# Optimization experiments

Measured on AMD Instinct MI355X. Metric: run time of the kernel, lower is better.

Reference implementation:

```python
import jax, jax.numpy as jnp
import numpy as np

MARGIN = 0.2
EPS = 1e-5
NEG_SENTINEL = -1e9


def _cos_sim(a, b):
    a = a / jnp.linalg.norm(a, axis=-1, keepdims=True)
    b = b / jnp.linalg.norm(b, axis=-1, keepdims=True)
    return a @ b.T  # [B, B]


def _row_losses(sm, labels):
    # sm: [B, B] similarity matrix; one loop body of the original, vectorized over rows i.
    diag = jnp.diagonal(sm)                      # pos_pair_ (scalar per row)
    pos_valid = diag < (1.0 - EPS)               # pos_pair_[pos_pair_ < 1-eps]
    neg_mask = labels[None, :] != labels[:, None]
    # neg_pair_[neg_pair_ + margin > min(pos_pair_)] ; min of a scalar is itself
    hard = neg_mask & ((sm + MARGIN) > diag[:, None])
    has_neg = jnp.any(hard, axis=1)
    neg_max = jnp.max(jnp.where(hard, sm, NEG_SENTINEL), axis=1)  # max(neg_pair)
    valid = pos_valid & has_neg
    pos_loss = jnp.maximum(0.2 * diag * diag - 0.7 * diag + 0.5, 0.0)
    neg_loss = jnp.maximum(0.9 * neg_max * neg_max - 0.4 * neg_max + 0.03, 0.0)
    return jnp.sum(jnp.where(valid, pos_loss + neg_loss, 0.0))


def setup_inputs() -> dict:
    key = jax.random.key(0)
    k1, k2 = jax.random.split(key)
    B, D = 8192, 256
    audio_embeds = jax.random.normal(k1, (B, D), dtype=jnp.float32)
    text_embeds = jax.random.normal(k2, (B, D), dtype=jnp.float32)
    labels = jnp.arange(B, dtype=jnp.int64)
    return {"audio_embeds": audio_embeds, "text_embeds": text_embeds, "labels": labels}


def reference(audio_embeds, text_embeds, labels):
    scores = _cos_sim(audio_embeds, text_embeds)  # [B, B]
    B = scores.shape[0]
    total = _row_losses(scores, labels) + _row_losses(scores.T, labels)
    return total / B
```

## Files before the change

kernel.cpp:

```cpp
#include <hip/hip_runtime.h>
#include <stdint.h>

#define BM 128
#define BN 128
#define KD 256

typedef __attribute__((ext_vector_type(4))) float f32x4;
typedef __attribute__((ext_vector_type(4))) int   i32x4;
typedef __attribute__((ext_vector_type(8))) int   i32x8;

__global__ __launch_bounds__(256) void norm_kernel(
    const float* __restrict__ a, const float* __restrict__ b,
    unsigned int* __restrict__ an, unsigned int* __restrict__ bn,
    float* __restrict__ diag, float* __restrict__ out, int D) {
  if (blockIdx.x == 0 && threadIdx.x == 0) out[0] = 0.f;
  const int row = blockIdx.x * 4 + (threadIdx.x >> 6);
  const int l = threadIdx.x & 63;
  const float4 av = ((const float4*)(a + (size_t)row * D))[l];
  const float4 bv = ((const float4*)(b + (size_t)row * D))[l];
  float ssa = av.x*av.x + av.y*av.y + av.z*av.z + av.w*av.w;
  float ssb = bv.x*bv.x + bv.y*bv.y + bv.z*bv.z + bv.w*bv.w;
  float dot = av.x*bv.x + av.y*bv.y + av.z*bv.z + av.w*bv.w;
  for (int off = 1; off < 64; off <<= 1) {
    ssa += __shfl_xor(ssa, off, 64);
    ssb += __shfl_xor(ssb, off, 64);
    dot += __shfl_xor(dot, off, 64);
  }
  const float inva = 1.0f / sqrtf(ssa);
  const float invb = 1.0f / sqrtf(ssb);
  if (l == 0) diag[row] = dot * inva * invb;
  int pa = 0, pb = 0;
  pa = __builtin_amdgcn_cvt_pk_fp8_f32(av.x * inva, av.y * inva, pa, 0);
  pa = __builtin_amdgcn_cvt_pk_fp8_f32(av.z * inva, av.w * inva, pa, 1);
  pb = __builtin_amdgcn_cvt_pk_fp8_f32(bv.x * invb, bv.y * invb, pb, 0);
  pb = __builtin_amdgcn_cvt_pk_fp8_f32(bv.z * invb, bv.w * invb, pb, 1);
  an[(size_t)row * (D / 4) + l] = (unsigned int)pa;
  bn[(size_t)row * (D / 4) + l] = (unsigned int)pb;
}

__global__ __launch_bounds__(512, 4) void gemm_max_kernel(
    const unsigned char* __restrict__ an, const unsigned char* __restrict__ bn,
    const int* __restrict__ labels,
    float* __restrict__ row_part, float* __restrict__ col_part, int B) {
  __shared__ __align__(16) unsigned char sA[2][BM * KD];
  __shared__ int lds_lab[8 * BM];
  __shared__ float lds_col[2][BN];

  const int tid  = threadIdx.x;
  const int lane = tid & 63;
  const int w    = tid >> 6;
  const int wm   = w >> 2, wn = w & 3;
  const int g0   = blockIdx.x >> 6;
  const int tj   = blockIdx.x & 63;

  const int sr = lane >> 4;
  const int sc = lane & 15;
  const int fr = lane & 15;
  const int hi = lane >> 4;
  const int p0 = ((2 * hi)     ^ (fr & 7)) * 16;
  const int p1 = ((2 * hi + 1) ^ (fr & 7)) * 16;

  auto stage = [&](int bsel, int k) {
    const int ti = g0 + 8 * k;
    #pragma unroll
    for (int pass = 0; pass < 4; ++pass) {
      const int r0  = pass * 32 + w * 4;
      const int row = r0 + sr;
      const int g = ((sc & 7) ^ (row & 7)) | (sc & 8);
      const unsigned char* ga = an + (size_t)(ti * BM + row) * KD + g * 16;
      __builtin_amdgcn_global_load_lds(
          (const __attribute__((address_space(1))) void*)ga,
          (__attribute__((address_space(3))) void*)(&sA[bsel][r0 * KD + lane * 16]),
          16, 0, 0);
    }
  };

  stage(0, 0);
  #pragma unroll
  for (int h = 0; h < 2; ++h) {
    const int i = h * 512 + tid;
    const int* gl = labels + g0 * 128 + (i >> 7) * 1024 + (i & 127);
    __builtin_amdgcn_global_load_lds(
        (const __attribute__((address_space(1))) void*)gl,
        (__attribute__((address_space(3))) void*)(&lds_lab[h * 512 + w * 64 + lane]),
        4, 0, 0);
  }
  i32x8 bfr[2][2];
  #pragma unroll
  for (int it = 0; it < 2; ++it)
    #pragma unroll
    for (int nt = 0; nt < 2; ++nt) {
      const unsigned char* gb =
          bn + (size_t)(tj * BN + wn * 32 + nt * 16 + fr) * KD + it * 128 + hi * 32;
      bfr[it][nt] = __builtin_shufflevector(*(const i32x4*)gb,
                                            *(const i32x4*)(gb + 16),
                                            0, 1, 2, 3, 4, 5, 6, 7);
    }
  const int labc0 = labels[tj * BN + wn * 32 + fr];
  const int labc1 = labels[tj * BN + wn * 32 + 16 + fr];
  __syncthreads();

  const int SC = 0x7F7F7F7F;
  float cp0 = -1e9f, cp1 = -1e9f;

  #pragma unroll
  for (int k = 0; k < 8; ++k) {
    if (k < 7) stage((k + 1) & 1, k + 1);

    f32x4 acc[4][2];
    #pragma unroll
    for (int mt = 0; mt < 4; ++mt) {
      acc[mt][0] = (f32x4){0.f, 0.f, 0.f, 0.f};
      acc[mt][1] = (f32x4){0.f, 0.f, 0.f, 0.f};
    }
    const unsigned char* Ab = sA[k & 1];
    #pragma unroll
    for (int it = 0; it < 2; ++it)
      #pragma unroll
      for (int mt = 0; mt < 4; ++mt) {
        const unsigned char* ra = Ab + (wm * 64 + mt * 16 + fr) * KD + it * 128;
        i32x8 af = __builtin_shufflevector(*(const i32x4*)(ra + p0),
                                           *(const i32x4*)(ra + p1),
                                           0, 1, 2, 3, 4, 5, 6, 7);
        acc[mt][0] = __builtin_amdgcn_mfma_scale_f32_16x16x128_f8f6f4(
            af, bfr[it][0], acc[mt][0], 0, 0, 0, SC, 0, SC);
        acc[mt][1] = __builtin_amdgcn_mfma_scale_f32_16x16x128_f8f6f4(
            af, bfr[it][1], acc[mt][1], 0, 0, 0, SC, 0, SC);
      }

    const size_t rowbase =
        (size_t)(tj * 4 + wn) * B + (size_t)(g0 + 8 * k) * BM + wm * 64;
    #pragma unroll
    for (int mt = 0; mt < 4; ++mt) {
      const i32x4 lv = *(const i32x4*)&lds_lab[k * 128 + wm * 64 + mt * 16 + hi * 4];
      float rr4[4];
      #pragma unroll
      for (int r = 0; r < 4; ++r) {
        const int l0 = lv[r];
        const float vm0 = (l0 != labc0) ? acc[mt][0][r] : -1e9f;
        const float vm1 = (l0 != labc1) ? acc[mt][1][r] : -1e9f;
        cp0 = fmaxf(cp0, vm0);
        cp1 = fmaxf(cp1, vm1);
        float rm = fmaxf(vm0, vm1);
        rm = fmaxf(rm, __shfl_xor(rm, 1, 64));
        rm = fmaxf(rm, __shfl_xor(rm, 2, 64));
        rm = fmaxf(rm, __shfl_xor(rm, 4, 64));
        rm = fmaxf(rm, __shfl_xor(rm, 8, 64));
        rr4[r] = rm;
      }
      if (fr == mt) {
        f32x4 v = {rr4[0], rr4[1], rr4[2], rr4[3]};
        *(f32x4*)(row_part + rowbase + mt * 16 + hi * 4) = v;
      }
    }

    __syncthreads();
  }

  float c0 = fmaxf(cp0, __shfl_xor(cp0, 16, 64));
  c0 = fmaxf(c0, __shfl_xor(c0, 32, 64));
  float c1 = fmaxf(cp1, __shfl_xor(cp1, 16, 64));
  c1 = fmaxf(c1, __shfl_xor(c1, 32, 64));
  if (hi == 0) {
    lds_col[wm][wn * 32 + fr] = c0;
    lds_col[wm][wn * 32 + 16 + fr] = c1;
  }
  __syncthreads();
  if (tid < BN)
    col_part[(size_t)g0 * B + tj * BN + tid] =
        fmaxf(lds_col[0][tid], lds_col[1][tid]);
}

__global__ __launch_bounds__(256) void finalize_kernel(
    const float* __restrict__ row_part, const float* __restrict__ col_part,
    const float* __restrict__ diag, int B, int Tr, int Tc,
    float* __restrict__ out) {
  const int ln = threadIdx.x & 63;
  const int q  = threadIdx.x >> 6;
  const int item = blockIdx.x * 64 + ln;
  const bool isrow = item < B;
  const int i = isrow ? item : item - B;
  const float* part = isrow ? row_part : col_part;
  const int T = isrow ? Tr : Tc;
  const int tpq = (T + 3) >> 2;
  const int t1 = min(T, (q + 1) * tpq);
  float m = -1e9f;
  for (int t = q * tpq; t < t1; ++t) m = fmaxf(m, part[(size_t)t * B + i]);
  __shared__ float smq[4][64];
  smq[q][ln] = m;
  __syncthreads();
  if (q == 0) {
    m = fmaxf(fmaxf(smq[0][ln], smq[1][ln]), fmaxf(smq[2][ln], smq[3][ln]));
    const float d = diag[i];
    float loss = 0.f;
    if ((d < 1.0f - 1e-5f) && (m + 0.2f > d)) {
      loss = fmaxf(0.2f * d * d - 0.7f * d + 0.5f, 0.f) +
             fmaxf(0.9f * m * m - 0.4f * m + 0.03f, 0.f);
    }
    for (int off = 1; off < 64; off <<= 1) loss += __shfl_xor(loss, off, 64);
    if (ln == 0) atomicAdd(out, loss / (float)B);
  }
}

extern "C" void kernel_launch(void* const* d_in, const int* in_sizes, int n_in,
                              void* d_out, int out_size, void* d_ws, size_t ws_size,
                              hipStream_t stream) {
  const float* a      = (const float*)d_in[0];
  const float* b      = (const float*)d_in[1];
  const int*   labels = (const int*)d_in[2];
  const int B = in_sizes[2];
  const int D = in_sizes[0] / B;
  const int Tr = (B / BN) * 4;
  const int Tc = 8;

  char* ws = (char*)d_ws;
  unsigned char* an = (unsigned char*)ws;
  unsigned char* bn = (unsigned char*)(ws + (size_t)B * D);
  float* diag     = (float*)(ws + (size_t)2 * B * D);
  float* row_part = diag + B;
  float* col_part = row_part + (size_t)Tr * B;

  norm_kernel<<<B / 4, 256, 0, stream>>>(a, b, (unsigned int*)an,
                                         (unsigned int*)bn, diag,
                                         (float*)d_out, D);

  gemm_max_kernel<<<(B / BM) / 8 * (B / BN), 512, 0, stream>>>(
      an, bn, labels, row_part, col_part, B);

  finalize_kernel<<<(2 * B) / 64, 256, 0, stream>>>(
      row_part, col_part, diag, B, Tr, Tc, (float*)d_out);
}
```

Measured before the change: 140.9 us.

## Give each block one output tile and compute the transposed product for row maxima

Each block now handles a single 128x128 tile instead of looping over 8 A-tiles with double-buffered LDS staging, so the grid grows eightfold and column partials cover all B/BM tiles. Row maxima come from a second MFMA that computes the transposed product, so lanes hold rows and need only two shuffles instead of four per element. This drops the per-row shuffle reductions and the double buffering but doubles MFMA work and increases column-partial traffic in finalize.

Result: slower. 153.2 us (+8.7%).

```diff
diff --git a/kernel.cpp b/kernel.cpp
--- a/kernel.cpp
+++ b/kernel.cpp
@@ -42,16 +42,15 @@
     const unsigned char* __restrict__ an, const unsigned char* __restrict__ bn,
     const int* __restrict__ labels,
     float* __restrict__ row_part, float* __restrict__ col_part, int B) {
-  __shared__ __align__(16) unsigned char sA[2][BM * KD];
-  __shared__ int lds_lab[8 * BM];
+  __shared__ __align__(16) unsigned char sA[BM * KD];
   __shared__ float lds_col[2][BN];
 
   const int tid  = threadIdx.x;
   const int lane = tid & 63;
   const int w    = tid >> 6;
   const int wm   = w >> 2, wn = w & 3;
-  const int g0   = blockIdx.x >> 6;
   const int tj   = blockIdx.x & 63;
+  const int ti   = blockIdx.x >> 6;
 
   const int sr = lane >> 4;
   const int sc = lane & 15;
@@ -60,31 +59,18 @@
   const int p0 = ((2 * hi)     ^ (fr & 7)) * 16;
   const int p1 = ((2 * hi + 1) ^ (fr & 7)) * 16;
 
-  auto stage = [&](int bsel, int k) {
-    const int ti = g0 + 8 * k;
-    #pragma unroll
-    for (int pass = 0; pass < 4; ++pass) {
-      const int r0  = pass * 32 + w * 4;
-      const int row = r0 + sr;
-      const int g = ((sc & 7) ^ (row & 7)) | (sc & 8);
-      const unsigned char* ga = an + (size_t)(ti * BM + row) * KD + g * 16;
-      __builtin_amdgcn_global_load_lds(
-          (const __attribute__((address_space(1))) void*)ga,
-          (__attribute__((address_space(3))) void*)(&sA[bsel][r0 * KD + lane * 16]),
-          16, 0, 0);
-    }
-  };
-
-  stage(0, 0);
-  #pragma unroll
-  for (int h = 0; h < 2; ++h) {
-    const int i = h * 512 + tid;
-    const int* gl = labels + g0 * 128 + (i >> 7) * 1024 + (i & 127);
+  #pragma unroll
+  for (int pass = 0; pass < 4; ++pass) {
+    const int r0  = pass * 32 + w * 4;
+    const int row = r0 + sr;
+    const int g = ((sc & 7) ^ (row & 7)) | (sc & 8);
+    const unsigned char* ga = an + (size_t)(ti * BM + row) * KD + g * 16;
     __builtin_amdgcn_global_load_lds(
-        (const __attribute__((address_space(1))) void*)gl,
-        (__attribute__((address_space(3))) void*)(&lds_lab[h * 512 + w * 64 + lane]),
-        4, 0, 0);
-  }
+        (const __attribute__((address_space(1))) void*)ga,
+        (__attribute__((address_space(3))) void*)(sA + r0 * KD + lane * 16),
+        16, 0, 0);
+  }
+
   i32x8 bfr[2][2];
   #pragma unroll
   for (int it = 0; it < 2; ++it)
@@ -96,78 +82,85 @@
                                             *(const i32x4*)(gb + 16),
                                             0, 1, 2, 3, 4, 5, 6, 7);
     }
+  __syncthreads();
+
+  const int SC = 0x7F7F7F7F;
+  f32x4 acc[4][2], at[4][2];
+  #pragma unroll
+  for (int mt = 0; mt < 4; ++mt)
+    #pragma unroll
+    for (int nt = 0; nt < 2; ++nt) {
+      acc[mt][nt] = (f32x4){0.f, 0.f, 0.f, 0.f};
+      at[mt][nt]  = (f32x4){0.f, 0.f, 0.f, 0.f};
+    }
+
+  #pragma unroll
+  for (int it = 0; it < 2; ++it)
+    #pragma unroll
+    for (int mt = 0; mt < 4; ++mt) {
+      const unsigned char* ra = sA + (wm * 64 + mt * 16 + fr) * KD + it * 128;
+      const i32x8 af = __builtin_shufflevector(*(const i32x4*)(ra + p0),
+                                               *(const i32x4*)(ra + p1),
+                                               0, 1, 2, 3, 4, 5, 6, 7);
+      acc[mt][0] = __builtin_amdgcn_mfma_scale_f32_16x16x128_f8f6f4(
+          af, bfr[it][0], acc[mt][0], 0, 0, 0, SC, 0, SC);
+      acc[mt][1] = __builtin_amdgcn_mfma_scale_f32_16x16x128_f8f6f4(
+          af, bfr[it][1], acc[mt][1], 0, 0, 0, SC, 0, SC);
+      at[mt][0] = __builtin_amdgcn_mfma_scale_f32_16x16x128_f8f6f4(
+          bfr[it][0], af, at[mt][0], 0, 0, 0, SC, 0, SC);
+      at[mt][1] = __builtin_amdgcn_mfma_scale_f32_16x16x128_f8f6f4(
+          bfr[it][1], af, at[mt][1], 0, 0, 0, SC, 0, SC);
+    }
+
   const int labc0 = labels[tj * BN + wn * 32 + fr];
   const int labc1 = labels[tj * BN + wn * 32 + 16 + fr];
-  __syncthreads();
-
-  const int SC = 0x7F7F7F7F;
+  i32x4 lv[4], labj[2];
+  int la[4];
+  #pragma unroll
+  for (int mt = 0; mt < 4; ++mt) {
+    lv[mt] = *(const i32x4*)&labels[ti * BM + wm * 64 + mt * 16 + hi * 4];
+    la[mt] = labels[ti * BM + wm * 64 + mt * 16 + fr];
+  }
+  #pragma unroll
+  for (int nt = 0; nt < 2; ++nt)
+    labj[nt] = *(const i32x4*)&labels[tj * BN + wn * 32 + nt * 16 + hi * 4];
+
   float cp0 = -1e9f, cp1 = -1e9f;
-
-  #pragma unroll
-  for (int k = 0; k < 8; ++k) {
-    if (k < 7) stage((k + 1) & 1, k + 1);
-
-    f32x4 acc[4][2];
-    #pragma unroll
-    for (int mt = 0; mt < 4; ++mt) {
-      acc[mt][0] = (f32x4){0.f, 0.f, 0.f, 0.f};
-      acc[mt][1] = (f32x4){0.f, 0.f, 0.f, 0.f};
-    }
-    const unsigned char* Ab = sA[k & 1];
-    #pragma unroll
-    for (int it = 0; it < 2; ++it)
+  #pragma unroll
+  for (int mt = 0; mt < 4; ++mt)
+    #pragma unroll
+    for (int r = 0; r < 4; ++r) {
+      const int l0 = lv[mt][r];
+      cp0 = fmaxf(cp0, (l0 != labc0) ? acc[mt][0][r] : -1e9f);
+      cp1 = fmaxf(cp1, (l0 != labc1) ? acc[mt][1][r] : -1e9f);
+    }
+  cp0 = fmaxf(cp0, __shfl_xor(cp0, 16, 64));
+  cp0 = fmaxf(cp0, __shfl_xor(cp0, 32, 64));
+  cp1 = fmaxf(cp1, __shfl_xor(cp1, 16, 64));
+  cp1 = fmaxf(cp1, __shfl_xor(cp1, 32, 64));
+  if (hi == 0) {
+    lds_col[wm][wn * 32 + fr] = cp0;
+    lds_col[wm][wn * 32 + 16 + fr] = cp1;
+  }
+
+  #pragma unroll
+  for (int mt = 0; mt < 4; ++mt) {
+    const int lam = la[mt];
+    float rm = -1e9f;
+    #pragma unroll
+    for (int nt = 0; nt < 2; ++nt)
       #pragma unroll
-      for (int mt = 0; mt < 4; ++mt) {
-        const unsigned char* ra = Ab + (wm * 64 + mt * 16 + fr) * KD + it * 128;
-        i32x8 af = __builtin_shufflevector(*(const i32x4*)(ra + p0),
-                                           *(const i32x4*)(ra + p1),
-                                           0, 1, 2, 3, 4, 5, 6, 7);
-        acc[mt][0] = __builtin_amdgcn_mfma_scale_f32_16x16x128_f8f6f4(
-            af, bfr[it][0], acc[mt][0], 0, 0, 0, SC, 0, SC);
-        acc[mt][1] = __builtin_amdgcn_mfma_scale_f32_16x16x128_f8f6f4(
-            af, bfr[it][1], acc[mt][1], 0, 0, 0, SC, 0, SC);
-      }
-
-    const size_t rowbase =
-        (size_t)(tj * 4 + wn) * B + (size_t)(g0 + 8 * k) * BM + wm * 64;
-    #pragma unroll
-    for (int mt = 0; mt < 4; ++mt) {
-      const i32x4 lv = *(const i32x4*)&lds_lab[k * 128 + wm * 64 + mt * 16 + hi * 4];
-      float rr4[4];
-      #pragma unroll
-      for (int r = 0; r < 4; ++r) {
-        const int l0 = lv[r];
-        const float vm0 = (l0 != labc0) ? acc[mt][0][r] : -1e9f;
-        const float vm1 = (l0 != labc1) ? acc[mt][1][r] : -1e9f;
-        cp0 = fmaxf(cp0, vm0);
-        cp1 = fmaxf(cp1, vm1);
-        float rm = fmaxf(vm0, vm1);
-        rm = fmaxf(rm, __shfl_xor(rm, 1, 64));
-        rm = fmaxf(rm, __shfl_xor(rm, 2, 64));
-        rm = fmaxf(rm, __shfl_xor(rm, 4, 64));
-        rm = fmaxf(rm, __shfl_xor(rm, 8, 64));
-        rr4[r] = rm;
-      }
-      if (fr == mt) {
-        f32x4 v = {rr4[0], rr4[1], rr4[2], rr4[3]};
-        *(f32x4*)(row_part + rowbase + mt * 16 + hi * 4) = v;
-      }
-    }
-
-    __syncthreads();
-  }
-
-  float c0 = fmaxf(cp0, __shfl_xor(cp0, 16, 64));
-  c0 = fmaxf(c0, __shfl_xor(c0, 32, 64));
-  float c1 = fmaxf(cp1, __shfl_xor(cp1, 16, 64));
-  c1 = fmaxf(c1, __shfl_xor(c1, 32, 64));
-  if (hi == 0) {
-    lds_col[wm][wn * 32 + fr] = c0;
-    lds_col[wm][wn * 32 + 16 + fr] = c1;
-  }
+      for (int r = 0; r < 4; ++r)
+        rm = fmaxf(rm, (lam != labj[nt][r]) ? at[mt][nt][r] : -1e9f);
+    rm = fmaxf(rm, __shfl_xor(rm, 16, 64));
+    rm = fmaxf(rm, __shfl_xor(rm, 32, 64));
+    if (hi == 0)
+      row_part[(size_t)(tj * 4 + wn) * B + ti * BM + wm * 64 + mt * 16 + fr] = rm;
+  }
+
   __syncthreads();
   if (tid < BN)
-    col_part[(size_t)g0 * B + tj * BN + tid] =
+    col_part[(size_t)ti * B + tj * BN + tid] =
         fmaxf(lds_col[0][tid], lds_col[1][tid]);
 }
 
@@ -211,7 +204,7 @@
   const int B = in_sizes[2];
   const int D = in_sizes[0] / B;
   const int Tr = (B / BN) * 4;
-  const int Tc = 8;
+  const int Tc = B / BM;
 
   char* ws = (char*)d_ws;
   unsigned char* an = (unsigned char*)ws;
@@ -224,7 +217,7 @@
                                          (unsigned int*)bn, diag,
                                          (float*)d_out, D);
 
-  gemm_max_kernel<<<(B / BM) / 8 * (B / BN), 512, 0, stream>>>(
+  gemm_max_kernel<<<(B / BM) * (B / BN), 512, 0, stream>>>(
       an, bn, labels, row_part, col_part, B);
 
   finalize_kernel<<<(2 * B) / 64, 256, 0, stream>>>(
```
